# Kernel tuning notes

Measured on AMD Instinct MI355X. Metric: run time of the kernel, lower is better.

## Reference

```python
import jax, jax.numpy as jnp
import numpy as np

D_MODEL = 1024
N_HEADS = 8
D_HEAD = 64
D_FF = 4096
LAMBDA_INIT = 0.8
EPS = 1e-5


def _ln(x, g, b):
    m = jnp.mean(x, axis=-1, keepdims=True)
    v = jnp.mean(jnp.square(x - m), axis=-1, keepdims=True)
    return (x - m) * jax.lax.rsqrt(v + EPS) * g + b


def setup_inputs() -> dict:
    key = jax.random.key(0)
    ks = jax.random.split(key, 24)
    D, H, Dh, F = D_MODEL, N_HEADS, D_HEAD, D_FF
    P = 2 * H * Dh  # projection width for q/k/v (== D here)
    s = lambda fan: 1.0 / np.sqrt(fan)
    inp = {
        'x': jax.random.normal(ks[0], (2, 2048, D), jnp.float32),
        'ln1_g': jnp.ones((D,), jnp.float32), 'ln1_b': jnp.zeros((D,), jnp.float32),
        'ln2_g': jnp.ones((D,), jnp.float32), 'ln2_b': jnp.zeros((D,), jnp.float32),
        'Wq': jax.random.normal(ks[1], (D, P), jnp.float32) * s(D), 'bq': jnp.zeros((P,), jnp.float32),
        'Wk': jax.random.normal(ks[2], (D, P), jnp.float32) * s(D), 'bk': jnp.zeros((P,), jnp.float32),
        'Wv': jax.random.normal(ks[3], (D, P), jnp.float32) * s(D), 'bv': jnp.zeros((P,), jnp.float32),
        'Wo': jax.random.normal(ks[4], (P, D), jnp.float32) * s(P), 'bo': jnp.zeros((D,), jnp.float32),
        'lq1': jax.random.normal(ks[5], (H, Dh), jnp.float32) * 0.1,
        'lk1': jax.random.normal(ks[6], (H, Dh), jnp.float32) * 0.1,
        'lq2': jax.random.normal(ks[7], (H, Dh), jnp.float32) * 0.1,
        'lk2': jax.random.normal(ks[8], (H, Dh), jnp.float32) * 0.1,
        'gn_w': jnp.ones((P,), jnp.float32), 'gn_b': jnp.zeros((P,), jnp.float32),
        'W1': jax.random.normal(ks[9], (D, F), jnp.float32) * s(D), 'b1': jnp.zeros((F,), jnp.float32),
        'Wg': jax.random.normal(ks[10], (F, F), jnp.float32) * s(F), 'bg': jnp.zeros((F,), jnp.float32),
        'W2': jax.random.normal(ks[11], (F, D), jnp.float32) * s(F), 'b2': jnp.zeros((D,), jnp.float32),
    }
    return inp


def reference(x, ln1_g, ln1_b, ln2_g, ln2_b, Wq, bq, Wk, bk, Wv, bv, Wo, bo,
              lq1, lk1, lq2, lk2, gn_w, gn_b, W1, b1, Wg, bg, W2, b2):
    B, S, D = x.shape
    H, Dh = N_HEADS, D_HEAD
    scale = 1.0 / np.sqrt(Dh)

    # --- differential attention sublayer (pre-norm) ---
    h = _ln(x, ln1_g, ln1_b)
    q = (h @ Wq + bq).reshape(B, S, H, 2, Dh)
    k = (h @ Wk + bk).reshape(B, S, H, 2, Dh)
    v = (h @ Wv + bv).reshape(B, S, H, 2 * Dh)

    A1 = jax.nn.softmax(jnp.einsum('bshd,bthd->bhst', q[..., 0, :], k[..., 0, :]) * scale, axis=-1)
    A2 = jax.nn.softmax(jnp.einsum('bshd,bthd->bhst', q[..., 1, :], k[..., 1, :]) * scale, axis=-1)

    lam = (jnp.exp(jnp.sum(lq1 * lk1, axis=-1))
           - jnp.exp(jnp.sum(lq2 * lk2, axis=-1)) + LAMBDA_INIT)  # [H]
    diff = A1 - lam[None, :, None, None] * A2                     # [B,H,S,S]
    o = jnp.einsum('bhst,bthe->bshe', diff, v)                    # [B,S,H,2*Dh]

    # headwise GroupNorm over the 2*Dh channels of each head
    mu = jnp.mean(o, axis=-1, keepdims=True)
    var = jnp.mean(jnp.square(o - mu), axis=-1, keepdims=True)
    o = (o - mu) * jax.lax.rsqrt(var + EPS)
    o = o * gn_w.reshape(H, 2 * Dh) + gn_b.reshape(H, 2 * Dh)
    o = o * (1.0 - LAMBDA_INIT)

    attn_out = o.reshape(B, S, 2 * H * Dh) @ Wo + bo
    x = x + attn_out

    # --- FFN sublayer: note source applies prenorm2 BEFORE residual split ---
    x = _ln(x, ln2_g, ln2_b)
    u = x @ W1 + b1
    u = u * jax.nn.silu(u @ Wg + bg)   # swiGLU gate
    return x + (u @ W2 + b2)
```

## Files before the change

### kernel.cpp

```cpp
#include <hip/hip_runtime.h>
#include <hip/hip_bf16.h>


typedef __attribute__((ext_vector_type(8))) __bf16 bf16x8;
typedef __attribute__((ext_vector_type(4))) float f32x4;

#define GAS __attribute__((address_space(1)))
#define LAS __attribute__((address_space(3)))

__device__ __forceinline__ unsigned short f2bf(float f) {
  unsigned u = __float_as_uint(f);
  u += 0x7fffu + ((u >> 16) & 1u);
  return (unsigned short)(u >> 16);
}
__device__ __forceinline__ float bf2f(unsigned short s) {
  return __uint_as_float(((unsigned)s) << 16);
}

__global__ __launch_bounds__(256)
void batched_transpose(const float* __restrict__ sWq, const float* __restrict__ sWk,
                       const float* __restrict__ sWv, const float* __restrict__ sWo,
                       const float* __restrict__ sW1, const float* __restrict__ sWg,
                       const float* __restrict__ sW2,
                       unsigned short* __restrict__ dstbase, float qscale) {
  const int id = blockIdx.x;
  const float* W;
  int K, N, t;
  size_t doff;
  float scale = 1.0f;
  if (id < 256)       { W = sWq; K = 1024; N = 1024; t = id;        doff = 0;        scale = qscale; }
  else if (id < 512)  { W = sWk; K = 1024; N = 1024; t = id - 256;  doff = 1048576;  }
  else if (id < 768)  { W = sWv; K = 1024; N = 1024; t = id - 512;  doff = 2097152;  }
  else if (id < 1024) { W = sWo; K = 1024; N = 1024; t = id - 768;  doff = 3145728;  }
  else if (id < 2048) { W = sW1; K = 1024; N = 4096; t = id - 1024; doff = 4194304;  }
  else if (id < 6144) { W = sWg; K = 4096; N = 4096; t = id - 2048; doff = 8388608;  }
  else                { W = sW2; K = 4096; N = 1024; t = id - 6144; doff = 25165824; }
  unsigned short* WT = dstbase + doff;
  const int nx = N >> 6;
  const int n0 = (t % nx) * 64, k0 = (t / nx) * 64;

  __shared__ float tile[64][65];
  const int tr = threadIdx.x >> 4, tc = (threadIdx.x & 15) * 4;
#pragma unroll
  for (int i = 0; i < 4; ++i) {
    const float4 v = *(const float4*)&W[(size_t)(k0 + tr + i * 16) * N + n0 + tc];
    tile[tr + i * 16][tc + 0] = v.x;
    tile[tr + i * 16][tc + 1] = v.y;
    tile[tr + i * 16][tc + 2] = v.z;
    tile[tr + i * 16][tc + 3] = v.w;
  }
  __syncthreads();
#pragma unroll
  for (int i = 0; i < 4; ++i) {
    const int n = tr + i * 16;
    ushort4 o;
    o.x = f2bf(tile[tc + 0][n] * scale);
    o.y = f2bf(tile[tc + 1][n] * scale);
    o.z = f2bf(tile[tc + 2][n] * scale);
    o.w = f2bf(tile[tc + 3][n] * scale);
    *(ushort4*)&WT[(size_t)(n0 + n) * K + k0 + tc] = o;
  }
}

__global__ void prep_bias(const float* __restrict__ bq, const float* __restrict__ bk,
                          const float* __restrict__ bv, float* __restrict__ out,
                          float qscale) {
  const int i = blockIdx.x * 256 + threadIdx.x;
  if (i < 1024) out[i] = bq[i] * qscale;
  else if (i < 2048) out[i] = bk[i - 1024];
  else out[i] = bv[i - 2048];
}

__global__ __launch_bounds__(256)
void kv_prep(const unsigned short* __restrict__ qkv, unsigned short* __restrict__ KP,
             unsigned short* __restrict__ VT) {
  __shared__ unsigned short tile[128][66];
  const int bh = blockIdx.y, b = bh >> 3, h = bh & 7;
  const int s0 = blockIdx.x * 64;
  const size_t inbase = (size_t)b * 2048 * 3072 + h * 128;
  const int tr = threadIdx.x >> 4, tc = (threadIdx.x & 15) * 8;
#pragma unroll
  for (int i = 0; i < 4; ++i) {
    const int s = s0 + tr + i * 16;
    *(uint4*)&KP[((size_t)bh * 2048 + s) * 128 + tc] =
        *(const uint4*)&qkv[inbase + (size_t)s * 3072 + 1024 + tc];
  }
#pragma unroll
  for (int i = 0; i < 4; ++i) {
    const int r = tr + i * 16;
    const uint4 v = *(const uint4*)&qkv[inbase + (size_t)(s0 + r) * 3072 + 2048 + tc];
    const unsigned short* pv = (const unsigned short*)&v;
#pragma unroll
    for (int jj = 0; jj < 8; ++jj) tile[tc + jj][r] = pv[jj];
  }
  __syncthreads();
  const int e = threadIdx.x >> 1, sh = (threadIdx.x & 1) * 32;
#pragma unroll
  for (int i = 0; i < 4; ++i) {
    ushort4 o0, o1;
    o0.x = tile[e][sh + i * 8 + 0]; o0.y = tile[e][sh + i * 8 + 1];
    o0.z = tile[e][sh + i * 8 + 2]; o0.w = tile[e][sh + i * 8 + 3];
    o1.x = tile[e][sh + i * 8 + 4]; o1.y = tile[e][sh + i * 8 + 5];
    o1.z = tile[e][sh + i * 8 + 6]; o1.w = tile[e][sh + i * 8 + 7];
    *(ushort4*)&VT[((size_t)bh * 128 + e) * 2048 + s0 + sh + i * 8] = o0;
    *(ushort4*)&VT[((size_t)bh * 128 + e) * 2048 + s0 + sh + i * 8 + 4] = o1;
  }
}

__global__ void lam_kernel(const float* __restrict__ lq1, const float* __restrict__ lk1,
                           const float* __restrict__ lq2, const float* __restrict__ lk2,
                           float* __restrict__ lam) {
  const int w = threadIdx.x >> 6, d = threadIdx.x & 63;
  float a = lq1[w * 64 + d] * lk1[w * 64 + d];
  float c = lq2[w * 64 + d] * lk2[w * 64 + d];
#pragma unroll
  for (int off = 32; off; off >>= 1) {
    a += __shfl_xor(a, off);
    c += __shfl_xor(c, off);
  }
  if (d == 0) lam[w] = __expf(a) - __expf(c) + 0.8f;
}

__global__ __launch_bounds__(256)
void ln_kernel(const float* __restrict__ x, const float* __restrict__ g,
               const float* __restrict__ bsh, unsigned short* __restrict__ obf) {
  __shared__ float red[16];
  const int row = blockIdx.x, tid = threadIdx.x;
  const float4 v = *(const float4*)&x[(size_t)row * 1024 + tid * 4];
  float s = v.x + v.y + v.z + v.w;
  float q = v.x * v.x + v.y * v.y + v.z * v.z + v.w * v.w;
#pragma unroll
  for (int off = 32; off; off >>= 1) {
    s += __shfl_xor(s, off);
    q += __shfl_xor(q, off);
  }
  if ((tid & 63) == 0) {
    red[tid >> 6] = s;
    red[8 + (tid >> 6)] = q;
  }
  __syncthreads();
  s = red[0] + red[1] + red[2] + red[3];
  q = red[8] + red[9] + red[10] + red[11];
  const float mean = s * (1.f / 1024.f);
  const float var = q * (1.f / 1024.f) - mean * mean;
  const float rstd = rsqrtf(var + 1e-5f);
  const float4 gg = *(const float4*)&g[tid * 4];
  const float4 bb = *(const float4*)&bsh[tid * 4];
  ushort4 o;
  o.x = f2bf((v.x - mean) * rstd * gg.x + bb.x);
  o.y = f2bf((v.y - mean) * rstd * gg.y + bb.y);
  o.z = f2bf((v.z - mean) * rstd * gg.z + bb.z);
  o.w = f2bf((v.w - mean) * rstd * gg.w + bb.w);
  *(ushort4*)&obf[(size_t)row * 1024 + tid * 4] = o;
}

template <int EPI>
__global__ __launch_bounds__(256)
void gemm128(const unsigned short* __restrict__ A,
             const unsigned short* __restrict__ BT,
             const float* __restrict__ bias,
             const float* __restrict__ resf,
             const unsigned short* __restrict__ resb,
             void* __restrict__ Cout, int M, int N, int K, float bscale) {
  __shared__ unsigned short lds[32768];
  const int tid = threadIdx.x;
  const int w = tid >> 6, ln = tid & 63, lg = ln >> 4, lc = ln & 15;
  const int wm = w >> 1, wn = w & 1;
  const int nwg = gridDim.x * gridDim.y;
  const int linear = blockIdx.y * gridDim.x + blockIdx.x;
  const int swzb = (linear & 7) * (nwg >> 3) + (linear >> 3);
  const int m0 = (swzb / gridDim.x) * 128, n0 = (swzb % gridDim.x) * 128;

  f32x4 acc[4][4];
#pragma unroll
  for (int i = 0; i < 4; ++i)
#pragma unroll
    for (int j = 0; j < 4; ++j) acc[i][j] = (f32x4)0.f;

  auto stage_half = [&](int tensor, int j, int hh) {
    const unsigned short* base = tensor ? BT : A;
    const int row0 = (tensor ? n0 : m0) + hh * 64;
    const int slot = tensor * 4 + (j & 1) * 2 + hh;
#pragma unroll
    for (int c = 0; c < 2; ++c) {
      const int chunk = w * 2 + c;
      const int L = chunk * 1024 + ln * 16;
      const int r = L >> 7, inner = L & 127;
      const char* src = (const char*)(base + (size_t)(row0 + r) * K + j * 64) +
                        (inner ^ ((r & 7) << 4));
      __builtin_amdgcn_global_load_lds((GAS void*)src,
          (LAS void*)((char*)lds + slot * 8192 + chunk * 1024), 16, 0, 0);
    }
  };
  auto read_a = [&](int j, int mf, int ks) -> bf16x8 {
    const int r = mf * 16 + lc;
    const int slot = (j & 1) * 2 + wm;
    const int cb = ks * 64 + lg * 16;
    return *(const bf16x8*)((const char*)lds + slot * 8192 + r * 128 +
                            (cb ^ ((r & 7) << 4)));
  };
  auto read_b = [&](int j, int nf, int ks) -> bf16x8 {
    const int R = wn * 64 + nf * 16 + lc;
    const int slot = 4 + (j & 1) * 2 + (R >> 6);
    const int r = R & 63;
    const int cb = ks * 64 + lg * 16;
    return *(const bf16x8*)((const char*)lds + slot * 8192 + r * 128 +
                            (cb ^ ((r & 7) << 4)));
  };

  const int nkt = K / 64;

  stage_half(0, 0, 0); stage_half(0, 0, 1);
  stage_half(1, 0, 0); stage_half(1, 0, 1);
  stage_half(1, 1, 0); stage_half(1, 1, 1);
  asm volatile("s_waitcnt vmcnt(0)" ::: "memory");
  __builtin_amdgcn_s_barrier();

  bf16x8 bfr[4][2];
  for (int it = 0; it < nkt / 2; ++it) {
    const int J = it * 2;
#pragma unroll
    for (int half = 0; half < 2; ++half) {
      const int jc = J + half;
#pragma unroll
      for (int q = 0; q < 2; ++q) {
        if (q == 0) {
#pragma unroll
          for (int nf = 0; nf < 4; ++nf)
#pragma unroll
            for (int ks = 0; ks < 2; ++ks) bfr[nf][ks] = read_b(jc, nf, ks);
        }
        bf16x8 afr[2][2];
#pragma unroll
        for (int mm = 0; mm < 2; ++mm)
#pragma unroll
          for (int ks = 0; ks < 2; ++ks) afr[mm][ks] = read_a(jc, q * 2 + mm, ks);
        if (half == 0) {
          if (q == 0) { stage_half(0, J + 1, 0); stage_half(0, J + 1, 1); }
          else if (J + 2 < nkt) { stage_half(1, J + 2, 0); stage_half(1, J + 2, 1); }
        } else {
          if (q == 0) { if (J + 2 < nkt) { stage_half(0, J + 2, 0); stage_half(0, J + 2, 1); } }
          else if (J + 3 < nkt) { stage_half(1, J + 3, 0); stage_half(1, J + 3, 1); }
        }
        if (q == 0) asm volatile("s_waitcnt lgkmcnt(8)" ::: "memory");
        __builtin_amdgcn_s_barrier();
        __builtin_amdgcn_s_setprio(1);
#pragma unroll
        for (int mm = 0; mm < 2; ++mm)
#pragma unroll
          for (int nf = 0; nf < 4; ++nf)
#pragma unroll
            for (int ks = 0; ks < 2; ++ks)
              acc[q * 2 + mm][nf] = __builtin_amdgcn_mfma_f32_16x16x32_bf16(
                  afr[mm][ks], bfr[nf][ks], acc[q * 2 + mm][nf], 0, 0, 0);
        __builtin_amdgcn_s_setprio(0);
        if (q == 1) {
          if ((half == 0 && J + 2 < nkt) || (half == 1 && J + 3 < nkt))
            asm volatile("s_waitcnt vmcnt(4)" ::: "memory");
          else
            asm volatile("s_waitcnt vmcnt(0)" ::: "memory");
        }
        __builtin_amdgcn_s_barrier();
      }
    }
  }

#pragma unroll
  for (int mf = 0; mf < 4; ++mf) {
#pragma unroll
    for (int nf = 0; nf < 4; ++nf) {
      const int c = n0 + wn * 64 + nf * 16 + lc;
      const float bc = bias[c] * bscale;
#pragma unroll
      for (int jj = 0; jj < 4; ++jj) {
        const int r = m0 + wm * 64 + mf * 16 + lg * 4 + jj;
        const size_t idx = (size_t)r * N + c;
        const float v = acc[mf][nf][jj] + bc;
        if (EPI == 1) {
          ((float*)Cout)[idx] = resf[idx] + v;
        } else if (EPI == 2) {
          ((float*)Cout)[idx] = bf2f(resb[idx]) + v;
        } else {
          ((unsigned short*)Cout)[idx] = f2bf(v);
        }
      }
    }
  }
}

template <int EPI>
__global__ __launch_bounds__(512)
void gemm256(const unsigned short* __restrict__ A,
             const unsigned short* __restrict__ BT,
             const float* __restrict__ bias,
             const unsigned short* __restrict__ gate_u,
             unsigned short* __restrict__ Cout, int M, int N, int K) {
  __shared__ unsigned short lds[65536];
  const int tid = threadIdx.x;
  const int w = tid >> 6, ln = tid & 63, lg = ln >> 4, lc = ln & 15;
  const int wm = w >> 2, wn = w & 3;
  const int nwg = gridDim.x * gridDim.y;
  const int linear = blockIdx.y * gridDim.x + blockIdx.x;
  const int swzb = (linear & 7) * (nwg >> 3) + (linear >> 3);
  const int m0 = (swzb / gridDim.x) * 256, n0 = (swzb % gridDim.x) * 256;

  f32x4 acc[8][4];
#pragma unroll
  for (int i = 0; i < 8; ++i)
#pragma unroll
    for (int j = 0; j < 4; ++j) acc[i][j] = (f32x4)0.f;

  auto stage_half = [&](int tensor, int j, int hh) {
    const unsigned short* base = tensor ? BT : A;
    const int row0 = (tensor ? n0 : m0) + hh * 128;
    const int slot = tensor * 4 + (j & 1) * 2 + hh;
#pragma unroll
    for (int c = 0; c < 2; ++c) {
      const int chunk = w * 2 + c;
      const int L = chunk * 1024 + ln * 16;
      const int r = L >> 7, inner = L & 127;
      const char* src = (const char*)(base + (size_t)(row0 + r) * K + j * 64) +
                        (inner ^ ((r & 7) << 4));
      __builtin_amdgcn_global_load_lds((GAS void*)src,
          (LAS void*)((char*)lds + slot * 16384 + chunk * 1024), 16, 0, 0);
    }
  };
  auto read_a = [&](int j, int mf, int ks) -> bf16x8 {
    const int r = mf * 16 + lc;
    const int slot = (j & 1) * 2 + wm;
    const int cb = ks * 64 + lg * 16;
    return *(const bf16x8*)((const char*)lds + slot * 16384 + r * 128 +
                            (cb ^ ((r & 7) << 4)));
  };
  auto read_b = [&](int j, int nf, int ks) -> bf16x8 {
    const int R = wn * 64 + nf * 16 + lc;
    const int slot = 4 + (j & 1) * 2 + (R >> 7);
    const int r = R & 127;
    const int cb = ks * 64 + lg * 16;
    return *(const bf16x8*)((const char*)lds + slot * 16384 + r * 128 +
                            (cb ^ ((r & 7) << 4)));
  };

  const int nkt = K / 64;

  stage_half(0, 0, 0); stage_half(0, 0, 1);
  stage_half(1, 0, 0); stage_half(1, 0, 1);
  stage_half(1, 1, 0); stage_half(1, 1, 1);
  asm volatile("s_waitcnt vmcnt(0)" ::: "memory");
  __builtin_amdgcn_s_barrier();

  bf16x8 bfr[4][2];
  for (int it = 0; it < nkt / 2; ++it) {
    const int J = it * 2;
#pragma unroll
    for (int half = 0; half < 2; ++half) {
      const int jc = J + half;
#pragma unroll
      for (int q = 0; q < 4; ++q) {
        if (q == 0) {
#pragma unroll
          for (int nf = 0; nf < 4; ++nf)
#pragma unroll
            for (int ks = 0; ks < 2; ++ks) bfr[nf][ks] = read_b(jc, nf, ks);
        }
        bf16x8 afr[2][2];
#pragma unroll
        for (int mm = 0; mm < 2; ++mm)
#pragma unroll
          for (int ks = 0; ks < 2; ++ks) afr[mm][ks] = read_a(jc, q * 2 + mm, ks);
        if (half == 0) {
          if (q == 0) stage_half(0, J + 1, 0);
          if (q == 1) stage_half(0, J + 1, 1);
          if (q == 2 && J + 2 < nkt) stage_half(1, J + 2, 0);
          if (q == 3 && J + 2 < nkt) stage_half(1, J + 2, 1);
        } else {
          if (q == 0 && J + 2 < nkt) stage_half(0, J + 2, 0);
          if (q == 1 && J + 2 < nkt) stage_half(0, J + 2, 1);
          if (q == 2 && J + 3 < nkt) stage_half(1, J + 3, 0);
          if (q == 3 && J + 3 < nkt) stage_half(1, J + 3, 1);
        }
        if (q == 0) asm volatile("s_waitcnt lgkmcnt(8)" ::: "memory");
        __builtin_amdgcn_s_barrier();
        __builtin_amdgcn_s_setprio(1);
#pragma unroll
        for (int mm = 0; mm < 2; ++mm)
#pragma unroll
          for (int nf = 0; nf < 4; ++nf)
#pragma unroll
            for (int ks = 0; ks < 2; ++ks)
              acc[q * 2 + mm][nf] = __builtin_amdgcn_mfma_f32_16x16x32_bf16(
                  afr[mm][ks], bfr[nf][ks], acc[q * 2 + mm][nf], 0, 0, 0);
        __builtin_amdgcn_s_setprio(0);
        if (q == 3) asm volatile("s_waitcnt vmcnt(4)" ::: "memory");
        __builtin_amdgcn_s_barrier();
      }
    }
  }

#pragma unroll
  for (int mf = 0; mf < 8; ++mf) {
#pragma unroll
    for (int nf = 0; nf < 4; ++nf) {
      const int c = n0 + wn * 64 + nf * 16 + lc;
      const float bc = bias[c];
#pragma unroll
      for (int jj = 0; jj < 4; ++jj) {
        const int r = m0 + wm * 128 + mf * 16 + lg * 4 + jj;
        const size_t idx = (size_t)r * N + c;
        const float v = acc[mf][nf][jj] + bc;
        if (EPI == 0) {
          Cout[idx] = f2bf(v);
        } else {
          const float uu = bf2f(gate_u[idx]);
          const float sw = v / (1.f + __expf(-v));
          Cout[idx] = f2bf(uu * sw);
        }
      }
    }
  }
}

__global__ __launch_bounds__(256)
void attn_kernel(const unsigned short* __restrict__ q,
                 const unsigned short* __restrict__ KP,
                 const unsigned short* __restrict__ VT,
                 const float* __restrict__ lam,
                 const float* __restrict__ gn_w, const float* __restrict__ gn_b,
                 unsigned short* __restrict__ o) {
  constexpr int S = 2048;
  constexpr int QS = 3072;
  __shared__ unsigned short k_tile[2][32 * 128];
  __shared__ unsigned short v_tile[2][128 * 32];
  __shared__ unsigned short p_lds[4][2][512];
  const int tid = threadIdx.x, w = tid >> 6, ln = tid & 63, lg = ln >> 4, lc = ln & 15;
  const int id = blockIdx.x;
  const int bh = (id & 7) + 8 * ((id >> 8) & 1);
  const int qt = (id >> 3) & 31;
  const int h = bh & 7, b = bh >> 3;
  const size_t chan = (size_t)b * S * QS + h * 128;
  const size_t ochan = (size_t)b * S * 1024 + h * 128;
  const size_t kpbase = (size_t)bh * S * 128;
  const size_t vtbase = (size_t)bh * 128 * S;
  const int qrow = qt * 64 + w * 16 + lc;

  bf16x8 qf[2][2];
#pragma unroll
  for (int p = 0; p < 2; ++p)
#pragma unroll
    for (int ks = 0; ks < 2; ++ks)
      qf[p][ks] = *(const bf16x8*)&q[chan + (size_t)qrow * QS + p * 64 + ks * 32 + lg * 8];

  f32x4 O[2][8];
#pragma unroll
  for (int p = 0; p < 2; ++p)
#pragma unroll
    for (int ef = 0; ef < 8; ++ef) O[p][ef] = (f32x4)0.f;
  float lsum[2][4];
#pragma unroll
  for (int p = 0; p < 2; ++p)
#pragma unroll
    for (int j = 0; j < 4; ++j) lsum[p][j] = 0.f;

  const int prd = ((lc * 64 + lg * 16) ^ ((lc & 7) << 4)) >> 1;

  auto stage = [&](int buf, int t0) {
#pragma unroll
    for (int c = 0; c < 2; ++c) {
      {
        const int L = (w * 2 + c) * 1024 + ln * 16;
        const int r = L >> 8, inner = L & 255;
        const char* src = (const char*)(KP + kpbase + (size_t)(t0 + r) * 128) +
                          (inner ^ ((r & 7) << 4));
        __builtin_amdgcn_global_load_lds((GAS void*)src,
            (LAS void*)((char*)&k_tile[buf][0] + (w * 2 + c) * 1024), 16, 0, 0);
      }
      {
        const int L = (w * 2 + c) * 1024 + ln * 16;
        const int e = L >> 6, inner = L & 63;
        const char* src = (const char*)(VT + vtbase + (size_t)e * S + t0) +
                          (inner ^ ((e & 3) << 4));
        __builtin_amdgcn_global_load_lds((GAS void*)src,
            (LAS void*)((char*)&v_tile[buf][0] + (w * 2 + c) * 1024), 16, 0, 0);
      }
    }
  };

  auto compute = [&](int buf) {
    const char* kb = (const char*)&k_tile[buf][0];
    const char* vb = (const char*)&v_tile[buf][0];
    bf16x8 vf[8];
#pragma unroll
    for (int ef = 0; ef < 8; ++ef) {
      const int e = ef * 16 + lc;
      vf[ef] = *(const bf16x8*)(vb + e * 64 + ((lg * 16) ^ ((e & 3) << 4)));
    }
#pragma unroll
    for (int p = 0; p < 2; ++p) {
      bf16x8 kf[2][2];
#pragma unroll
      for (int tf = 0; tf < 2; ++tf) {
        const int r = tf * 16 + lc;
#pragma unroll
        for (int ks = 0; ks < 2; ++ks)
          kf[tf][ks] = *(const bf16x8*)(kb + r * 256 +
                          ((p * 128 + ks * 64 + lg * 16) ^ ((r & 7) << 4)));
      }
      f32x4 sfr[2];
      __builtin_amdgcn_s_setprio(1);
#pragma unroll
      for (int tf = 0; tf < 2; ++tf) {
        f32x4 acc = (f32x4)0.f;
#pragma unroll
        for (int ks = 0; ks < 2; ++ks)
          acc = __builtin_amdgcn_mfma_f32_16x16x32_bf16(qf[p][ks], kf[tf][ks], acc, 0, 0, 0);
        sfr[tf] = acc;
      }
      __builtin_amdgcn_s_setprio(0);

#pragma unroll
      for (int tf = 0; tf < 2; ++tf)
#pragma unroll
        for (int j = 0; j < 4; ++j) {
          const float e = __expf(sfr[tf][j]);
          lsum[p][j] += e;
          const int qq = lg * 4 + j;
          const int wi = ((qq * 64 + (tf * 16 + lc) * 2) ^ ((qq & 7) << 4)) >> 1;
          p_lds[w][p][wi] = f2bf(e);
        }

      const bf16x8 pa = *(const bf16x8*)&p_lds[w][p][prd];
      __builtin_amdgcn_s_setprio(1);
#pragma unroll
      for (int ef = 0; ef < 8; ++ef)
        O[p][ef] = __builtin_amdgcn_mfma_f32_16x16x32_bf16(pa, vf[ef], O[p][ef], 0, 0, 0);
      __builtin_amdgcn_s_setprio(0);
    }
  };

  stage(0, 0);
  int cur = 0;
  for (int it = 0; it < 64; ++it) {
    if (it < 63) {
      stage(cur ^ 1, (it + 1) * 32);
      asm volatile("s_waitcnt vmcnt(4)" ::: "memory");
    } else {
      asm volatile("s_waitcnt vmcnt(0)" ::: "memory");
    }
    __builtin_amdgcn_s_barrier();
    compute(cur);
    __builtin_amdgcn_s_barrier();
    cur ^= 1;
  }

#pragma unroll
  for (int p = 0; p < 2; ++p)
#pragma unroll
    for (int j = 0; j < 4; ++j) {
      float s = lsum[p][j];
      s += __shfl_xor(s, 1);
      s += __shfl_xor(s, 2);
      s += __shfl_xor(s, 4);
      s += __shfl_xor(s, 8);
      lsum[p][j] = s;
    }
  const float lamh = lam[h];
#pragma unroll
  for (int j = 0; j < 4; ++j) {
    const float inv1 = 1.f / lsum[0][j];
    const float inv2 = lamh / lsum[1][j];
    float dv[8], sum = 0.f, sq = 0.f;
#pragma unroll
    for (int ef = 0; ef < 8; ++ef) {
      dv[ef] = O[0][ef][j] * inv1 - O[1][ef][j] * inv2;
      sum += dv[ef];
      sq += dv[ef] * dv[ef];
    }
    sum += __shfl_xor(sum, 1); sq += __shfl_xor(sq, 1);
    sum += __shfl_xor(sum, 2); sq += __shfl_xor(sq, 2);
    sum += __shfl_xor(sum, 4); sq += __shfl_xor(sq, 4);
    sum += __shfl_xor(sum, 8); sq += __shfl_xor(sq, 8);
    const float mean = sum * (1.f / 128.f);
    const float var = sq * (1.f / 128.f) - mean * mean;
    const float rstd = rsqrtf(var + 1e-5f);
    const int row = qt * 64 + w * 16 + lg * 4 + j;
#pragma unroll
    for (int ef = 0; ef < 8; ++ef) {
      const int e = ef * 16 + lc;
      const float val = (dv[ef] - mean) * rstd * gn_w[h * 128 + e] + gn_b[h * 128 + e];
      o[ochan + (size_t)row * 1024 + e] = f2bf(val * 0.2f);
    }
  }
}

extern "C" void kernel_launch(void* const* d_in, const int* in_sizes, int n_in,
                              void* d_out, int out_size, void* d_ws, size_t ws_size,
                              hipStream_t stream) {
  (void)in_sizes; (void)n_in; (void)out_size; (void)ws_size;
  const float* x    = (const float*)d_in[0];
  const float* ln1g = (const float*)d_in[1];
  const float* ln1b = (const float*)d_in[2];
  const float* ln2g = (const float*)d_in[3];
  const float* ln2b = (const float*)d_in[4];
  const float* Wq   = (const float*)d_in[5];
  const float* bq   = (const float*)d_in[6];
  const float* Wk   = (const float*)d_in[7];
  const float* bk   = (const float*)d_in[8];
  const float* Wv   = (const float*)d_in[9];
  const float* bv   = (const float*)d_in[10];
  const float* Wo   = (const float*)d_in[11];
  const float* bo   = (const float*)d_in[12];
  const float* lq1  = (const float*)d_in[13];
  const float* lk1  = (const float*)d_in[14];
  const float* lq2  = (const float*)d_in[15];
  const float* lk2  = (const float*)d_in[16];
  const float* gnw  = (const float*)d_in[17];
  const float* gnb  = (const float*)d_in[18];
  const float* W1   = (const float*)d_in[19];
  const float* b1   = (const float*)d_in[20];
  const float* Wg   = (const float*)d_in[21];
  const float* bg   = (const float*)d_in[22];
  const float* W2   = (const float*)d_in[23];
  const float* b2   = (const float*)d_in[24];

  const int B = 2, S = 2048, D = 1024, F = 4096;
  const int M = B * S;
  const float qscale = 0.125f;

  char* ws = (char*)d_ws;
  size_t off = 0;
  auto alloc = [&](size_t bytes) {
    char* p = ws + off;
    off += (bytes + 255) & ~(size_t)255;
    return p;
  };
  unsigned short* WqkvT = (unsigned short*)alloc((size_t)3 * D * D * 2);
  unsigned short* WoT = (unsigned short*)alloc((size_t)D * D * 2);
  unsigned short* W1T = (unsigned short*)alloc((size_t)F * D * 2);
  unsigned short* WgT = (unsigned short*)alloc((size_t)F * F * 2);
  unsigned short* W2T = (unsigned short*)alloc((size_t)D * F * 2);
  float*          lamw= (float*)alloc(256);
  float*          bqkv= (float*)alloc(3072 * 4);
  unsigned short* h_bf= (unsigned short*)alloc((size_t)M * D * 2);
  unsigned short* qkv = (unsigned short*)alloc((size_t)M * 3 * D * 2);
  unsigned short* o_bf= (unsigned short*)alloc((size_t)M * D * 2);
  float*          x1  = (float*)alloc((size_t)M * D * 4);
  unsigned short* x2b = (unsigned short*)alloc((size_t)M * D * 2);
  unsigned short* u_bf= (unsigned short*)alloc((size_t)M * F * 2);
  unsigned short* w_bf= h_bf;

  unsigned short* KP = (unsigned short*)x1;
  unsigned short* VT = u_bf + (size_t)12 * 1024 * 1024;

  batched_transpose<<<7168, 256, 0, stream>>>(Wq, Wk, Wv, Wo, W1, Wg, W2, WqkvT, qscale);
  prep_bias<<<12, 256, 0, stream>>>(bq, bk, bv, bqkv, qscale);
  lam_kernel<<<1, 512, 0, stream>>>(lq1, lk1, lq2, lk2, lamw);

  ln_kernel<<<M, 256, 0, stream>>>(x, ln1g, ln1b, h_bf);
  gemm256<0><<<dim3(3 * D / 256, M / 256), 512, 0, stream>>>(h_bf, WqkvT, bqkv, nullptr, qkv, M, 3 * D, D);
  kv_prep<<<dim3(S / 64, 16), 256, 0, stream>>>(qkv, KP, VT);
  attn_kernel<<<dim3(512), 256, 0, stream>>>(qkv, KP, VT, lamw, gnw, gnb, o_bf);
  gemm128<1><<<dim3(D / 128, M / 128), 256, 0, stream>>>(o_bf, WoT, bo, x, nullptr, x1, M, D, D, 1.0f);

  ln_kernel<<<M, 256, 0, stream>>>(x1, ln2g, ln2b, x2b);
  gemm256<0><<<dim3(F / 256, M / 256), 512, 0, stream>>>(x2b, W1T, b1, nullptr, u_bf, M, F, D);
  gemm256<2><<<dim3(F / 256, M / 256), 512, 0, stream>>>(u_bf, WgT, bg, u_bf, w_bf, M, F, F);
  gemm128<2><<<dim3(D / 128, M / 128), 256, 0, stream>>>(w_bf, W2T, b2, nullptr, x2b, (float*)d_out, M, D, F, 1.0f);
}
```

Before: 400.2 us.

## Fold bias prep into transpose kernel, tighten GEMM waits, restructure attention PV loop

Merges the bias-preparation kernel into the batched weight transpose launch as extra blocks, removing one kernel launch. In both GEMM kernels, the per-wave partial LDS waitcnt before the barrier is replaced by a full lgkmcnt(0) wait after the barrier plus a sched_barrier, which changes how fragment loads are ordered relative to the MFMAs. In attention, both P tiles are computed first, then V fragments are loaded in two halves of four, so fewer V registers are live at once. The full LDS wait may serialize work that used to overlap with compute, and the attention reorder trades register pressure against load latency.

```diff
diff --git a/kernel.cpp b/kernel.cpp
--- a/kernel.cpp
+++ b/kernel.cpp
@@ -22,8 +22,18 @@
                        const float* __restrict__ sWv, const float* __restrict__ sWo,
                        const float* __restrict__ sW1, const float* __restrict__ sWg,
                        const float* __restrict__ sW2,
-                       unsigned short* __restrict__ dstbase, float qscale) {
+                       unsigned short* __restrict__ dstbase,
+                       const float* __restrict__ bq, const float* __restrict__ bk,
+                       const float* __restrict__ bv, float* __restrict__ bqkv,
+                       float qscale) {
   const int id = blockIdx.x;
+  if (id >= 7168) {
+    const int i = (id - 7168) * 256 + threadIdx.x;
+    if (i < 1024) bqkv[i] = bq[i] * qscale;
+    else if (i < 2048) bqkv[i] = bk[i - 1024];
+    else bqkv[i] = bv[i - 2048];
+    return;
+  }
   const float* W;
   int K, N, t;
   size_t doff;
@@ -60,15 +70,6 @@
     o.w = f2bf(tile[tc + 3][n] * scale);
     *(ushort4*)&WT[(size_t)(n0 + n) * K + k0 + tc] = o;
   }
-}
-
-__global__ void prep_bias(const float* __restrict__ bq, const float* __restrict__ bk,
-                          const float* __restrict__ bv, float* __restrict__ out,
-                          float qscale) {
-  const int i = blockIdx.x * 256 + threadIdx.x;
-  if (i < 1024) out[i] = bq[i] * qscale;
-  else if (i < 2048) out[i] = bk[i - 1024];
-  else out[i] = bv[i - 2048];
 }
 
 __global__ __launch_bounds__(256)
@@ -242,8 +243,9 @@
           if (q == 0) { if (J + 2 < nkt) { stage_half(0, J + 2, 0); stage_half(0, J + 2, 1); } }
           else if (J + 3 < nkt) { stage_half(1, J + 3, 0); stage_half(1, J + 3, 1); }
         }
-        if (q == 0) asm volatile("s_waitcnt lgkmcnt(8)" ::: "memory");
         __builtin_amdgcn_s_barrier();
+        asm volatile("s_waitcnt lgkmcnt(0)" ::: "memory");
+        __builtin_amdgcn_sched_barrier(0);
         __builtin_amdgcn_s_setprio(1);
 #pragma unroll
         for (int mm = 0; mm < 2; ++mm)
@@ -379,8 +381,9 @@
           if (q == 2 && J + 3 < nkt) stage_half(1, J + 3, 0);
           if (q == 3 && J + 3 < nkt) stage_half(1, J + 3, 1);
         }
-        if (q == 0) asm volatile("s_waitcnt lgkmcnt(8)" ::: "memory");
         __builtin_amdgcn_s_barrier();
+        asm volatile("s_waitcnt lgkmcnt(0)" ::: "memory");
+        __builtin_amdgcn_sched_barrier(0);
         __builtin_amdgcn_s_setprio(1);
 #pragma unroll
         for (int mm = 0; mm < 2; ++mm)
@@ -488,12 +491,6 @@
   auto compute = [&](int buf) {
     const char* kb = (const char*)&k_tile[buf][0];
     const char* vb = (const char*)&v_tile[buf][0];
-    bf16x8 vf[8];
-#pragma unroll
-    for (int ef = 0; ef < 8; ++ef) {
-      const int e = ef * 16 + lc;
-      vf[ef] = *(const bf16x8*)(vb + e * 64 + ((lg * 16) ^ ((e & 3) << 4)));
-    }
 #pragma unroll
     for (int p = 0; p < 2; ++p) {
       bf16x8 kf[2][2];
@@ -516,7 +513,6 @@
         sfr[tf] = acc;
       }
       __builtin_amdgcn_s_setprio(0);
-
 #pragma unroll
       for (int tf = 0; tf < 2; ++tf)
 #pragma unroll
@@ -527,12 +523,26 @@
           const int wi = ((qq * 64 + (tf * 16 + lc) * 2) ^ ((qq & 7) << 4)) >> 1;
           p_lds[w][p][wi] = f2bf(e);
         }
-
-      const bf16x8 pa = *(const bf16x8*)&p_lds[w][p][prd];
+    }
+    bf16x8 pa[2];
+#pragma unroll
+    for (int p = 0; p < 2; ++p)
+      pa[p] = *(const bf16x8*)&p_lds[w][p][prd];
+#pragma unroll
+    for (int half = 0; half < 2; ++half) {
+      bf16x8 vf[4];
+#pragma unroll
+      for (int ef = 0; ef < 4; ++ef) {
+        const int e = (half * 4 + ef) * 16 + lc;
+        vf[ef] = *(const bf16x8*)(vb + e * 64 + ((lg * 16) ^ ((e & 3) << 4)));
+      }
       __builtin_amdgcn_s_setprio(1);
 #pragma unroll
-      for (int ef = 0; ef < 8; ++ef)
-        O[p][ef] = __builtin_amdgcn_mfma_f32_16x16x32_bf16(pa, vf[ef], O[p][ef], 0, 0, 0);
+      for (int p = 0; p < 2; ++p)
+#pragma unroll
+        for (int ef = 0; ef < 4; ++ef)
+          O[p][half * 4 + ef] = __builtin_amdgcn_mfma_f32_16x16x32_bf16(
+              pa[p], vf[ef], O[p][half * 4 + ef], 0, 0, 0);
       __builtin_amdgcn_s_setprio(0);
     }
   };
@@ -651,8 +661,8 @@
   unsigned short* KP = (unsigned short*)x1;
   unsigned short* VT = u_bf + (size_t)12 * 1024 * 1024;
 
-  batched_transpose<<<7168, 256, 0, stream>>>(Wq, Wk, Wv, Wo, W1, Wg, W2, WqkvT, qscale);
-  prep_bias<<<12, 256, 0, stream>>>(bq, bk, bv, bqkv, qscale);
+  batched_transpose<<<7180, 256, 0, stream>>>(Wq, Wk, Wv, Wo, W1, Wg, W2, WqkvT,
+                                              bq, bk, bv, bqkv, qscale);
   lam_kernel<<<1, 512, 0, stream>>>(lq1, lk1, lq2, lk2, lamw);
 
   ln_kernel<<<M, 256, 0, stream>>>(x, ln1g, ln1b, h_bf);
```

After: 390.7 us. 2.4% less time.
